# Optimization experiments

Hardware: AMD Instinct MI355X
Metric: run time of the kernel (lower is better)

The kernel has to match this reference:

```python
import jax, jax.numpy as jnp
import numpy as np

N_NODES = 100000
N_EDGES = 1600000
IN_C, OUT_C, HEADS = 128, 32, 4


def setup_inputs() -> dict:
    key = jax.random.key(0)
    k1, k2, k3, k4 = jax.random.split(key, 4)
    x = jax.random.normal(k1, (N_NODES, IN_C), dtype=jnp.float32)
    edge_index = jax.random.randint(k2, (2, N_EDGES), 0, N_NODES, dtype=jnp.int64)
    # xavier-uniform-ish scaled params
    w_bound = float(np.sqrt(6.0 / (IN_C + OUT_C)))
    W = jax.random.uniform(k3, (HEADS, IN_C, OUT_C), dtype=jnp.float32,
                           minval=-w_bound, maxval=w_bound)
    a_bound = float(np.sqrt(6.0 / (2 * OUT_C + 1)))
    a = jax.random.uniform(k4, (HEADS, 2 * OUT_C), dtype=jnp.float32,
                           minval=-a_bound, maxval=a_bound)
    return {"x": x, "edge_index": edge_index, "W": W, "a": a}


def reference(x, edge_index, W, a):
    N = x.shape[0]
    out_c = W.shape[-1]
    src, dst = edge_index[0], edge_index[1]
    # node transform: [N, H, O]
    h = jnp.einsum('ni,hio->nho', x, W)
    h_src = h[src]            # [E, H, O] gather
    h_dst = h[dst]            # [E, H, O] gather
    # a = [a_src | a_dst]; avoids materializing concatenated edge features
    a_src, a_dst = a[:, :out_c], a[:, out_c:]
    e = (jnp.einsum('eho,ho->eh', h_src, a_src)
         + jnp.einsum('eho,ho->eh', h_dst, a_dst))
    e = jax.nn.leaky_relu(e, negative_slope=0.2)  # [E, H]
    # segment softmax over dst groups (stable: subtract per-segment max)
    seg_max = jax.ops.segment_max(e, dst, num_segments=N)   # [N, H]
    e_exp = jnp.exp(e - seg_max[dst])
    seg_sum = jax.ops.segment_sum(e_exp, dst, num_segments=N)  # [N, H]
    alpha = e_exp / seg_sum[dst]  # each present segment has denom >= 1
    # dropout is identity in eval mode
    msg = alpha[..., None] * h_src              # [E, H, O]
    out = jax.ops.segment_sum(msg, dst, num_segments=N)  # [N, H, O]
    return out.reshape(N, -1)  # concat=True -> [N, H*O]
```

## Files before the change

kernel.cpp:

```cpp
#include <hip/hip_runtime.h>
#include <hip/hip_fp16.h>

using f32x4  = __attribute__((ext_vector_type(4))) float;
using short8 = __attribute__((ext_vector_type(8))) short;
using ushort8 = __attribute__((ext_vector_type(8))) unsigned short;

#define LOG2E 1.4426950408889634f
#define TP 136

static __device__ __forceinline__ unsigned short f2bf(float f) {
  union { float f; unsigned u; } c; c.f = f;
  unsigned u = c.u;
  return (unsigned short)((u + 0x7fffu + ((u >> 16) & 1u)) >> 16);
}
static __device__ __forceinline__ float bf2f(unsigned short b) {
  union { unsigned u; float f; } c; c.u = ((unsigned)b) << 16;
  return c.f;
}

__global__ __launch_bounds__(256) void k_wz(const float* __restrict__ W,
                                            unsigned short* __restrict__ wt,
                                            int* __restrict__ cnt, int N) {
  int idx = blockIdx.x * 256 + threadIdx.x;
  if (idx < 16384) {
    int hh = idx >> 12, i = (idx >> 5) & 127, o = idx & 31;
    wt[(hh * 32 + o) * 128 + i] = f2bf(W[idx]);
  }
  for (int j = idx; j < N; j += gridDim.x * 256) cnt[j] = 0;
}

__global__ __launch_bounds__(256) void k_gp(const float* __restrict__ x,
                                            const unsigned short* __restrict__ wt,
                                            const float* __restrict__ a,
                                            const void* __restrict__ ei,
                                            unsigned short* __restrict__ hbf,
                                            float* __restrict__ ssrc,
                                            float* __restrict__ sdst,
                                            int* __restrict__ cnt,
                                            int* __restrict__ slots,
                                            int nnodes, int E, int NG, int C) {
  __shared__ __align__(16) unsigned short tr[64 * TP];
  __shared__ int sh_is64;
  const int tid = threadIdx.x;
  const unsigned bI = blockIdx.x;

  int gemm_bid = -1, prep_bid;
  if (bI < 5u * (unsigned)NG) {
    unsigned q = bI / 5u, r = bI % 5u;
    if (r == 0) gemm_bid = (int)q;
    prep_bid = (int)(4u * q + r - 1u);
  } else {
    prep_bid = (int)(4u * (unsigned)NG + (bI - 5u * (unsigned)NG));
  }

  if (gemm_bid >= 0) {
    const int n0 = gemm_bid * 64;
    const int wave = tid >> 6, lane = tid & 63;
    const int m0 = wave * 16;
    const int lr = lane & 15, lh = lane >> 4;
    const int n = n0 + m0 + lr;
    const bool rowok = n < nnodes;
    const float* xrow = x + (size_t)n * 128;

    short8 avf[4];
#pragma unroll
    for (int kk = 0; kk < 4; ++kk) {
      float4 u0 = make_float4(0.f, 0.f, 0.f, 0.f), u1 = u0;
      if (rowok) {
        u0 = *(const float4*)(xrow + kk * 32 + lh * 8);
        u1 = *(const float4*)(xrow + kk * 32 + lh * 8 + 4);
      }
      short8 v;
      v[0] = (short)f2bf(u0.x); v[1] = (short)f2bf(u0.y);
      v[2] = (short)f2bf(u0.z); v[3] = (short)f2bf(u0.w);
      v[4] = (short)f2bf(u1.x); v[5] = (short)f2bf(u1.y);
      v[6] = (short)f2bf(u1.z); v[7] = (short)f2bf(u1.w);
      avf[kk] = v;
    }

    f32x4 acc[8] = {};
#pragma unroll
    for (int kk = 0; kk < 4; ++kk) {
#pragma unroll
      for (int f = 0; f < 8; ++f) {
        short8 bv = *(const short8*)(wt + (f * 16 + lr) * 128 + kk * 32 + lh * 8);
        acc[f] = __builtin_amdgcn_mfma_f32_16x16x32_bf16(avf[kk], bv, acc[f], 0, 0, 0);
      }
    }

#pragma unroll
    for (int j = 0; j < 4; ++j) {
      int rr = m0 + lh * 4 + j;
#pragma unroll
      for (int f = 0; f < 8; ++f) tr[rr * TP + f * 16 + lr] = f2bf(acc[f][j]);
    }

    float avc[4][4];
#pragma unroll
    for (int hh = 0; hh < 4; ++hh) {
      avc[hh][0] = a[hh * 64 + lr];
      avc[hh][1] = a[hh * 64 + 16 + lr];
      avc[hh][2] = a[hh * 64 + 32 + lr];
      avc[hh][3] = a[hh * 64 + 48 + lr];
    }
#pragma unroll
    for (int j = 0; j < 4; ++j) {
      int nn = n0 + m0 + lh * 4 + j;
#pragma unroll
      for (int hh = 0; hh < 4; ++hh) {
        float s0 = acc[2 * hh][j] * avc[hh][0] + acc[2 * hh + 1][j] * avc[hh][1];
        float s1 = acc[2 * hh][j] * avc[hh][2] + acc[2 * hh + 1][j] * avc[hh][3];
#pragma unroll
        for (int m = 1; m < 16; m <<= 1) {
          s0 += __shfl_xor(s0, m);
          s1 += __shfl_xor(s1, m);
        }
        if (lr == hh && nn < nnodes) {
          ssrc[(size_t)nn * 4 + hh] = s0 * LOG2E;
          sdst[(size_t)nn * 4 + hh] = s1 * LOG2E;
        }
      }
    }

    __syncthreads();
#pragma unroll
    for (int it = 0; it < 4; ++it) {
      int idx = tid + it * 256;
      int r = idx >> 4, c16 = idx & 15;
      int nn = n0 + r;
      if (nn < nnodes)
        *(ushort8*)(hbf + (size_t)nn * 128 + c16 * 8) = *(const ushort8*)&tr[r * TP + c16 * 8];
    }
  } else {
    if (tid < 64) {
      long long v = ((const long long*)ei)[tid];
      int ok = (v >= 0 && v < (long long)nnodes) ? 1 : 0;
      unsigned long long m = __ballot(ok);
      if (tid == 0) sh_is64 = (m == ~0ull) ? 1 : 0;
    }
    __syncthreads();
    const int is64 = sh_is64;
    int e = prep_bid * 256 + tid;
    if (e < E) {
      int s, d;
      if (is64) {
        s = (int)((const long long*)ei)[e];
        d = (int)((const long long*)ei)[(size_t)E + e];
      } else {
        s = ((const int*)ei)[e];
        d = ((const int*)ei)[(size_t)E + e];
      }
      int pos = atomicAdd(&cnt[d], 1);
      if (pos < C) slots[d * C + pos] = s;
    }
  }
}

__global__ __launch_bounds__(256) void k_gather(const unsigned short* __restrict__ hbf,
                                                const int* __restrict__ cntArr,
                                                const int* __restrict__ slots,
                                                const float* __restrict__ ssrc,
                                                const float* __restrict__ sdst,
                                                float* __restrict__ out, int N, int C) {
  int wid = (blockIdx.x * 256 + threadIdx.x) >> 6;
  int lane = threadIdx.x & 63;
  if (wid >= N) return;
  const int dst = wid;
  int cv = cntArr[dst];
  if (cv > C) cv = C;
  const int beg = dst * C;
  const int end = beg + cv;
  const int half = lane >> 5;
  const int sl = lane & 31;
  const int hh4 = sl >> 3;
  const int lq = lane & 3;
  const int le = lane >> 2;
  if (cv == 0) {
    if (half == 0)
      *(float4*)(out + (size_t)dst * 128 + sl * 4) = make_float4(0.f, 0.f, 0.f, 0.f);
    return;
  }
  const float sdP = sdst[(size_t)dst * 4 + lq];
  const uint2* __restrict__ h2 = (const uint2*)hbf;
  float a0 = 0.f, a1 = 0.f, a2 = 0.f, a3 = 0.f, ps = 0.f;

  for (int i = beg; i < end; i += 16) {
    int ipe = i + le;
    bool pok = ipe < end;
    int ipc = pok ? ipe : (end - 1);
    int sP = slots[ipc];
    float ev = ssrc[(size_t)sP * 4 + lq] + sdP;
    ev = fmaxf(ev, 0.2f * ev);
    float pv = pok ? exp2f(ev) : 0.f;

    uint2 hv[8];
#pragma unroll
    for (int k = 0; k < 8; ++k) {
      int ek = i + half * 8 + k;
      int ec = (ek < end) ? ek : (end - 1);
      int s = slots[ec];
      hv[k] = h2[((unsigned)s << 5) | (unsigned)sl];
    }
    float pk[8];
#pragma unroll
    for (int k = 0; k < 8; ++k)
      pk[k] = __shfl(pv, ((half * 8 + k) << 2) | hh4);
#pragma unroll
    for (int k = 0; k < 8; ++k) {
      unsigned lo = hv[k].x, hi = hv[k].y;
      a0 += pk[k] * bf2f((unsigned short)(lo & 0xffff));
      a1 += pk[k] * bf2f((unsigned short)(lo >> 16));
      a2 += pk[k] * bf2f((unsigned short)(hi & 0xffff));
      a3 += pk[k] * bf2f((unsigned short)(hi >> 16));
      ps += pk[k];
    }
  }
  a0 += __shfl_xor(a0, 32);
  a1 += __shfl_xor(a1, 32);
  a2 += __shfl_xor(a2, 32);
  a3 += __shfl_xor(a3, 32);
  ps += __shfl_xor(ps, 32);
  float r = (ps > 0.f) ? 1.f / ps : 0.f;
  if (half == 0) {
    float4 o = make_float4(a0 * r, a1 * r, a2 * r, a3 * r);
    *(float4*)(out + (size_t)dst * 128 + sl * 4) = o;
  }
}

extern "C" void kernel_launch(void* const* d_in, const int* in_sizes, int n_in,
                              void* d_out, int out_size, void* d_ws, size_t ws_size,
                              hipStream_t stream) {
  const float* x = (const float*)d_in[0];
  const void*  ei = d_in[1];
  const float* W = (const float*)d_in[2];
  const float* a = (const float*)d_in[3];
  float* out = (float*)d_out;

  const int N = in_sizes[0] / 128;
  const int E = in_sizes[1] / 2;
  const int NB = (N + 255) / 256;
  const int NG = (N + 63) / 64;
  const int NP = (E + 255) / 256;
  const int extra = (NP > 4 * NG) ? (NP - 4 * NG) : 0;
  const int TOT = 5 * NG + extra;

  char* ws = (char*)d_ws;
  unsigned short* hbf = (unsigned short*)ws;             ws += (size_t)N * 128 * 2;
  unsigned short* wt  = (unsigned short*)ws;             ws += 16384 * 2;
  float* ssrc     = (float*)ws;                          ws += (size_t)N * 4 * 4;
  float* sdst     = (float*)ws;                          ws += (size_t)N * 4 * 4;
  int*   cnt      = (int*)ws;                            ws += (size_t)N * 4;
  int*   slots    = (int*)ws;

  size_t used = (size_t)(ws - (char*)d_ws);
  size_t avail = (ws_size > used) ? (ws_size - used) : 0;
  int C = (int)(avail / ((size_t)N * 4));
  if (C > 64) C = 64;

  k_wz<<<NB, 256, 0, stream>>>(W, wt, cnt, N);
  k_gp<<<TOT, 256, 0, stream>>>(x, wt, a, ei, hbf, ssrc, sdst, cnt, slots, N, E, NG, C);
  k_gather<<<(N + 3) / 4, 256, 0, stream>>>(hbf, cnt, slots, ssrc, sdst, out, N, C);
}
```

Measured before the change: 166.2 us.

## Partition edge bucketing by destination range across persistent prep blocks

Replaces the one-edge-per-thread bucketing blocks with a fixed pool of 1024 prep worker-block positions, each split into 8 partitions. Every partition scans all destination indices and handles only the edges whose destination falls in its eighth of the node range. Prep and GEMM blocks are interleaved in a new 8:8 pattern. The goal is to localize the atomics and slot writes so the counters and slot lists of each partition stay resident in cache. In exchange, the destination array is read 8 times and the source loads become scattered.

```diff
diff --git a/kernel.cpp b/kernel.cpp
--- a/kernel.cpp
+++ b/kernel.cpp
@@ -38,22 +38,23 @@
                                             float* __restrict__ sdst,
                                             int* __restrict__ cnt,
                                             int* __restrict__ slots,
-                                            int nnodes, int E, int NG, int C) {
+                                            int nnodes, int E, int NG, int NP, int C) {
   __shared__ __align__(16) unsigned short tr[64 * TP];
   __shared__ int sh_is64;
   const int tid = threadIdx.x;
   const unsigned bI = blockIdx.x;
-
-  int gemm_bid = -1, prep_bid;
-  if (bI < 5u * (unsigned)NG) {
-    unsigned q = bI / 5u, r = bI % 5u;
-    if (r == 0) gemm_bid = (int)q;
-    prep_bid = (int)(4u * q + r - 1u);
+  const unsigned INT = 2u * (unsigned)NP;
+
+  int gemm_bid = -1, prep_part = -1, prep_wblk = 0;
+  if (bI < INT) {
+    unsigned q = bI >> 4, r = bI & 15u;
+    if (r < 8u) { prep_part = (int)r; prep_wblk = (int)q; }
+    else gemm_bid = (int)(q * 8u + (r - 8u));
   } else {
-    prep_bid = (int)(4u * (unsigned)NG + (bI - 5u * (unsigned)NG));
-  }
-
-  if (gemm_bid >= 0) {
+    gemm_bid = (int)(NP + (bI - INT));
+  }
+
+  if (gemm_bid >= 0 && gemm_bid < NG) {
     const int n0 = gemm_bid * 64;
     const int wave = tid >> 6, lane = tid & 63;
     const int m0 = wave * 16;
@@ -131,7 +132,7 @@
       if (nn < nnodes)
         *(ushort8*)(hbf + (size_t)nn * 128 + c16 * 8) = *(const ushort8*)&tr[r * TP + c16 * 8];
     }
-  } else {
+  } else if (prep_part >= 0) {
     if (tid < 64) {
       long long v = ((const long long*)ei)[tid];
       int ok = (v >= 0 && v < (long long)nnodes) ? 1 : 0;
@@ -140,18 +141,33 @@
     }
     __syncthreads();
     const int is64 = sh_is64;
-    int e = prep_bid * 256 + tid;
-    if (e < E) {
-      int s, d;
-      if (is64) {
-        s = (int)((const long long*)ei)[e];
-        d = (int)((const long long*)ei)[(size_t)E + e];
-      } else {
-        s = ((const int*)ei)[e];
-        d = ((const int*)ei)[(size_t)E + e];
-      }
-      int pos = atomicAdd(&cnt[d], 1);
-      if (pos < C) slots[d * C + pos] = s;
+    const int lo = (int)(((long long)nnodes * prep_part) >> 3);
+    const int hi = (int)(((long long)nnodes * (prep_part + 1)) >> 3);
+    const int nwb = NP >> 3;
+    const int stride = nwb * 256;
+    const int* ei32 = (const int*)ei;
+    const int base = prep_wblk * 256 + tid;
+
+    for (int e0 = base; e0 < E; e0 += 4 * stride) {
+      int dv[4]; bool okk[4];
+#pragma unroll
+      for (int k = 0; k < 4; ++k) {
+        int e = e0 + k * stride;
+        okk[k] = e < E;
+        dv[k] = 0;
+        if (okk[k])
+          dv[k] = is64 ? ei32[2 * ((size_t)E + e)]
+                       : ei32[(size_t)E + e];
+      }
+#pragma unroll
+      for (int k = 0; k < 4; ++k) {
+        if (okk[k] && dv[k] >= lo && dv[k] < hi) {
+          int e = e0 + k * stride;
+          int s = is64 ? (int)((const long long*)ei)[e] : ei32[e];
+          int pos = atomicAdd(&cnt[dv[k]], 1);
+          if (pos < C) slots[dv[k] * C + pos] = s;
+        }
+      }
     }
   }
 }
@@ -240,9 +256,10 @@
   const int E = in_sizes[1] / 2;
   const int NB = (N + 255) / 256;
   const int NG = (N + 63) / 64;
-  const int NP = (E + 255) / 256;
-  const int extra = (NP > 4 * NG) ? (NP - 4 * NG) : 0;
-  const int TOT = 5 * NG + extra;
+  const int NP = 1024;
+  const int INT = 2 * NP;
+  const int tail = (NG > NP) ? (NG - NP) : 0;
+  const int TOT = INT + tail;
 
   char* ws = (char*)d_ws;
   unsigned short* hbf = (unsigned short*)ws;             ws += (size_t)N * 128 * 2;
@@ -258,6 +275,6 @@
   if (C > 64) C = 64;
 
   k_wz<<<NB, 256, 0, stream>>>(W, wt, cnt, N);
-  k_gp<<<TOT, 256, 0, stream>>>(x, wt, a, ei, hbf, ssrc, sdst, cnt, slots, N, E, NG, C);
+  k_gp<<<TOT, 256, 0, stream>>>(x, wt, a, ei, hbf, ssrc, sdst, cnt, slots, N, E, NG, NP, C);
   k_gather<<<(N + 3) / 4, 256, 0, stream>>>(hbf, cnt, slots, ssrc, sdst, out, N, C);
 }
```

Result: slower. 176.8 us (+6.4%).
